# Kernel tuning notes

Hardware: AMD Instinct MI355X
Metric: run time of the kernel (lower is better)

Reference implementation:

```python
import jax, jax.numpy as jnp
import numpy as np

CONF = 0.25
IOU = 0.7
MAX_DET = 300
IMG_H = 1280
IMG_W = 1280
KPT_SHAPE = (17, 3)
MAX_NMS = 3000
BS = 16
N_ANCH = 33600  # (1280/8)^2 + (1280/16)^2 + (1280/32)^2


def setup_inputs() -> dict:
    key = jax.random.key(0)
    k1, k2, k3, k4 = jax.random.split(key, 4)
    # realistic YOLO head outputs: centers in image, positive w/h, conf in (0,1)
    cxy = jax.random.uniform(k1, (BS, 2, N_ANCH)) * jnp.array([IMG_W, IMG_H], jnp.float32).reshape(1, 2, 1)
    wh = jax.random.uniform(k2, (BS, 2, N_ANCH)) * 200.0 + 4.0
    conf = jax.random.uniform(k3, (BS, 1, N_ANCH))
    kpts = jax.random.uniform(k4, (BS, 51, N_ANCH)) * float(IMG_W)
    preds = jnp.concatenate([cxy, wh, conf, kpts], axis=1).astype(jnp.float32)
    return {"preds": preds}


def _pairwise_iou(boxes):
    # boxes: [M, 4] xyxy
    area = (boxes[:, 2] - boxes[:, 0]) * (boxes[:, 3] - boxes[:, 1])
    lt = jnp.maximum(boxes[:, None, :2], boxes[None, :, :2])
    rb = jnp.minimum(boxes[:, None, 2:], boxes[None, :, 2:])
    wh = jnp.clip(rb - lt, 0.0)
    inter = wh[..., 0] * wh[..., 1]
    return inter / (area[:, None] + area[None, :] - inter + 1e-9)


def _nms_keep(boxes, valid):
    # greedy NMS over score-descending boxes; returns bool keep mask [M]
    M = boxes.shape[0]
    idx = jnp.arange(M)
    supp = (_pairwise_iou(boxes) > IOU) & (idx[None, :] > idx[:, None])

    def body(i, keep):
        # row i suppresses later boxes only if it is itself kept
        return keep & ~(supp[i] & keep[i])

    return jax.lax.fori_loop(0, M, body, valid)


def _per_image(boxes_xywh, scores, kpts):
    # boxes_xywh: [N,4], scores: [N], kpts: [N,51]
    valid = scores > CONF
    masked = jnp.where(valid, scores, -1.0)
    order = jnp.argsort(-masked)[:MAX_NMS]  # top max_nms by score, desc
    b = boxes_xywh[order]
    sc = scores[order]
    kp = kpts[order]
    v = valid[order]
    # xywh -> xyxy with clip to image bounds
    cx, cy, w, h = b[:, 0], b[:, 1], b[:, 2], b[:, 3]
    x1 = jnp.clip(cx - w / 2, 0.0, IMG_W)
    y1 = jnp.clip(cy - h / 2, 0.0, IMG_H)
    x2 = jnp.clip(cx + w / 2, 0.0, IMG_W)
    y2 = jnp.clip(cy + h / 2, 0.0, IMG_H)
    bxy = jnp.stack([x1, y1, x2, y2], axis=-1)
    # faithful to original _clip_coords quirk: only channels 0 and 1 of the 51 clipped
    kp = kp.at[:, 0].set(jnp.clip(kp[:, 0], 0.0, IMG_W))
    kp = kp.at[:, 1].set(jnp.clip(kp[:, 1], 0.0, IMG_H))
    keep = _nms_keep(bxy, v)
    rank = jnp.cumsum(keep) - 1
    sel = keep & (rank < MAX_DET)
    tgt = jnp.where(sel, rank, MAX_DET)  # dropped rows scatter to slot MAX_DET (sliced off)
    ob = jnp.zeros((MAX_DET + 1, 4), bxy.dtype).at[tgt].set(jnp.where(sel[:, None], bxy, 0.0))[:MAX_DET]
    osc = jnp.zeros((MAX_DET + 1, 1), sc.dtype).at[tgt].set(jnp.where(sel[:, None], sc[:, None], 0.0))[:MAX_DET]
    okp = jnp.zeros((MAX_DET + 1, 51), kp.dtype).at[tgt].set(jnp.where(sel[:, None], kp, 0.0))[:MAX_DET]
    return ob, osc, okp


def reference(preds):
    bs = preds.shape[0]
    x = jnp.transpose(preds, (0, 2, 1))  # [bs, N, 56]
    ob, osc, okp = jax.vmap(_per_image)(x[..., :4], x[..., 4], x[..., 5:])
    return ob, osc, okp.reshape(bs, MAX_DET, *KPT_SHAPE)
```

## Files before the change

### kernel.cpp

```cpp
#include <hip/hip_runtime.h>
#include <stdint.h>

#define N_ANCH 33600
#define BS 16
#define NCH 56
#define MAX_NMS 3000
#define MAX_DET 300
#define CONF_T 0.25f
#define IOU_T 0.7f
#define IMG 1280.0f
#define NW 47
#define NBINS 4096
#define HIST_BINS 4097
#define S_STRIDE 4104
#define CAP 4096

#define OFF_CURS 0
#define OFF_KEPT (OFF_CURS + BS*NBINS*4)
#define ZERO_BYTES (OFF_KEPT + 64)
#define OFF_HIST  ZERO_BYTES
#define OFF_START (OFF_HIST + BS*S_STRIDE*4)
#define OFF_B     (OFF_START + BS*S_STRIDE*4)
#define OFF_M     (OFF_B + 64)
#define OFF_CAND  (OFF_M + 64)
#define OFF_SORT  (OFF_CAND + BS*CAP*8)
#define OFF_OIDX  (OFF_SORT + BS*CAP*8)
#define OFF_SC    (OFF_OIDX + BS*MAX_NMS*4)
#define OFF_BOX   (OFF_SC + BS*MAX_NMS*4)
#define OFF_SEL   (OFF_BOX + BS*MAX_NMS*16)

__device__ __forceinline__ int score_bucket(float c, uint32_t* bits_out) {
    if (!(c > CONF_T)) { *bits_out = 0u; return 0; }
    uint32_t bits = __float_as_uint(c);
    *bits_out = bits;
    int bucket = (int)(bits >> 12) - 0x3E800 + 1;
    bucket = bucket < 1 ? 1 : (bucket > NBINS ? NBINS : bucket);
    return bucket;
}

__global__ void k_histscan(const float* __restrict__ preds, int* __restrict__ hist,
                           int* __restrict__ start, int* __restrict__ Bthr,
                           int* __restrict__ Mout) {
    __shared__ int hl[HIST_BINS];
    __shared__ int part[256];
    __shared__ int suf[256];
    int b = blockIdx.x, t = threadIdx.x;
    for (int i = t; i < HIST_BINS; i += 1024) hl[i] = 0;
    __syncthreads();
    const float* conf = preds + (size_t)b * NCH * N_ANCH + 4 * N_ANCH;
    for (int a = t; a < N_ANCH; a += 1024) {
        uint32_t bits;
        int bucket = score_bucket(conf[a], &bits);
        if (bucket > 0) atomicAdd(&hl[bucket], 1);
    }
    __syncthreads();
    if (t < 256) {
        int s = 0;
        for (int k = 0; k < 16; k++) s += hl[1 + t * 16 + k];
        part[t] = s;
    }
    __syncthreads();
    if (t == 0) {
        int run = 0;
        for (int i = 255; i >= 0; i--) { suf[i] = run; run += part[i]; }
        if (run < MAX_NMS) { Bthr[b] = 1; Mout[b] = run; }
    }
    __syncthreads();
    if (t < 256) {
        int run = suf[t];
        bool maycross = (run < MAX_NMS) && (run + part[t] >= MAX_NMS);
        bool done = false;
        for (int k = 15; k >= 0; k--) {
            int bin = 1 + t * 16 + k;
            start[b * S_STRIDE + bin] = run;
            hist[b * S_STRIDE + bin] = hl[bin];
            run += hl[bin];
            if (maycross && !done && run >= MAX_NMS) {
                Bthr[b] = bin; Mout[b] = run; done = true;
            }
        }
    }
}

__global__ void k_scatter(const float* __restrict__ preds, const int* __restrict__ Bthr,
                          const int* __restrict__ start, int* __restrict__ curs,
                          unsigned long long* __restrict__ cand) {
    int g = blockIdx.x * blockDim.x + threadIdx.x;
    if (g >= BS * N_ANCH) return;
    int b = g / N_ANCH, a = g - b * N_ANCH;
    float c = preds[(size_t)b * NCH * N_ANCH + 4 * N_ANCH + a];
    uint32_t bits;
    int bucket = score_bucket(c, &bits);
    if (bucket > 0 && bucket >= Bthr[b]) {
        int pos = start[b * S_STRIDE + bucket] + atomicAdd(&curs[b * NBINS + (bucket - 1)], 1);
        if (pos < CAP)
            cand[b * CAP + pos] =
                ((unsigned long long)bits << 32) | (uint32_t)(~(uint32_t)a);
    }
}

__global__ void k_rank(const int* __restrict__ Bthr, const int* __restrict__ start,
                       const int* __restrict__ hist,
                       const unsigned long long* __restrict__ cand,
                       unsigned long long* __restrict__ sorted) {
    int wid = (blockIdx.x * blockDim.x + threadIdx.x) >> 6;
    int lane = threadIdx.x & 63;
    if (wid >= BS * NBINS) return;
    int b = wid >> 12;
    int bin = (wid & (NBINS - 1)) + 1;
    if (bin < Bthr[b]) return;
    int s = start[b * S_STRIDE + bin];
    if (s >= MAX_NMS) return;
    int n = hist[b * S_STRIDE + bin];
    if (n <= 0) return;
    if (s + n > CAP) n = CAP - s;
    const unsigned long long* seg = cand + b * CAP + s;
    unsigned long long* oseg = sorted + b * CAP + s;
    for (int e = lane; e < n; e += 64) {
        unsigned long long ke = seg[e];
        int r = 0;
        for (int j = 0; j < n; j++) r += (seg[j] > ke);
        oseg[r] = ke;
    }
}

__global__ void k_gather(const float* __restrict__ preds,
                         const unsigned long long* __restrict__ sorted,
                         const int* __restrict__ M,
                         int* __restrict__ oidx, float* __restrict__ sc_out,
                         float4* __restrict__ box_out) {
    int g = blockIdx.x * blockDim.x + threadIdx.x;
    if (g >= BS * MAX_NMS) return;
    int b = g / MAX_NMS, p = g - b * MAX_NMS;
    float score; float4 bx; int oi;
    if (p < M[b]) {
        unsigned long long key = sorted[b * CAP + p];
        const float* pr = preds + (size_t)b * NCH * N_ANCH;
        oi = (int)(~(uint32_t)key);
        score = __uint_as_float((uint32_t)(key >> 32));
        float cx = pr[0 * N_ANCH + oi], cy = pr[1 * N_ANCH + oi];
        float w  = pr[2 * N_ANCH + oi], h  = pr[3 * N_ANCH + oi];
        bx.x = fminf(fmaxf(cx - w * 0.5f, 0.f), IMG);
        bx.y = fminf(fmaxf(cy - h * 0.5f, 0.f), IMG);
        bx.z = fminf(fmaxf(cx + w * 0.5f, 0.f), IMG);
        bx.w = fminf(fmaxf(cy + h * 0.5f, 0.f), IMG);
    } else {
        oi = 0; score = -1.0f; bx = make_float4(0.f, 0.f, 0.f, 0.f);
    }
    oidx[b * MAX_NMS + p] = oi;
    sc_out[b * MAX_NMS + p] = score;
    box_out[b * MAX_NMS + p] = bx;
}

__device__ __forceinline__ float iou_pair(float4 bi, float ai, float4 bj) {
    float aj  = (bj.z - bj.x) * (bj.w - bj.y);
    float ltx = fmaxf(bi.x, bj.x), lty = fmaxf(bi.y, bj.y);
    float rbx = fminf(bi.z, bj.z), rby = fminf(bi.w, bj.w);
    float wx  = fmaxf(rbx - ltx, 0.f), wy = fmaxf(rby - lty, 0.f);
    float inter = wx * wy;
    return inter / (ai + aj - inter + 1e-9f);
}

__device__ __forceinline__ unsigned long long readlane64(unsigned long long v, int lane) {
    uint32_t lo = (uint32_t)v, hi = (uint32_t)(v >> 32);
    uint32_t rlo = __builtin_amdgcn_readlane(lo, lane);
    uint32_t rhi = __builtin_amdgcn_readlane(hi, lane);
    return ((unsigned long long)rhi << 32) | (unsigned long long)rlo;
}

__global__ void k_nms(const float4* __restrict__ box_ws, const float* __restrict__ sc_ws,
                      int* __restrict__ sel_slot, int* __restrict__ kept_count) {
    __shared__ float4 lbox[MAX_NMS];
    __shared__ float4 kbox[MAX_DET];
    __shared__ float  karea[MAX_DET];
    __shared__ unsigned long long pres[NW];
    __shared__ unsigned long long diag[64];
    __shared__ unsigned long long keptmask_sh;
    int b = blockIdx.x, t = threadIdx.x;
    if (t < NW) pres[t] = 0ull;
    __syncthreads();
    for (int j = t; j < MAX_NMS; j += 1024) {
        lbox[j] = box_ws[b * MAX_NMS + j];
        if (!(sc_ws[b * MAX_NMS + j] > CONF_T))
            atomicOr(&pres[j >> 6], 1ull << (j & 63));
    }
    __syncthreads();
    int kc = 0;
    for (int c = 0; c < NW && kc < MAX_DET; c++) {
        int base = c * 64;
        if (t < 64) diag[t] = 0ull;
        __syncthreads();
        {
            int jl = t >> 4, kk = t & 15;
            int j = base + jl;
            if (j < MAX_NMS && kc > 0) {
                float4 bj = lbox[j];
                bool sup = false;
                for (int kidx = kk; kidx < kc; kidx += 16) {
                    if (iou_pair(kbox[kidx], karea[kidx], bj) > IOU_T) { sup = true; break; }
                }
                if (sup) atomicOr(&pres[c], 1ull << jl);
            }
        }
        {
            int il = t >> 4;
            int j0 = (t & 15) * 4;
            int i = base + il;
            if (i < MAX_NMS) {
                float4 bi = lbox[i];
                float ai = (bi.z - bi.x) * (bi.w - bi.y);
                unsigned long long m = 0ull;
                for (int q = 0; q < 4; q++) {
                    int jl = j0 + q, j = base + jl;
                    if (j > i && j < MAX_NMS) {
                        if (iou_pair(bi, ai, lbox[j]) > IOU_T) m |= 1ull << jl;
                    }
                }
                if (m) atomicOr(&diag[il], m);
            }
        }
        __syncthreads();
        if (t < 64) {
            unsigned long long mydiag = diag[t];
            unsigned long long s = pres[c];
            unsigned long long keptm = 0ull;
            int room = MAX_DET - kc;
            int jmax = MAX_NMS - base; if (jmax > 64) jmax = 64;
            for (int bb = 0; bb < jmax; bb++) {
                if (!((s >> bb) & 1ull)) {
                    s |= readlane64(mydiag, bb);
                    keptm |= 1ull << bb;
                    if (--room == 0) break;
                }
            }
            if (t == 0) keptmask_sh = keptm;
        }
        __syncthreads();
        unsigned long long keptm = keptmask_sh;
        if (t < 64 && ((keptm >> t) & 1ull)) {
            int pos = kc + __popcll(keptm & ((1ull << t) - 1ull));
            float4 bx = lbox[base + t];
            kbox[pos] = bx;
            karea[pos] = (bx.z - bx.x) * (bx.w - bx.y);
            sel_slot[b * MAX_DET + pos] = base + t;
        }
        kc += __popcll(keptm);
        __syncthreads();
    }
    if (t == 0) kept_count[b] = kc;
}

__global__ void k_out(const float* __restrict__ preds, const float4* __restrict__ box_ws,
                      const float* __restrict__ sc_ws, const int* __restrict__ oidx,
                      const int* __restrict__ sel_slot, const int* __restrict__ kept_count,
                      float* __restrict__ out) {
    int g = blockIdx.x * blockDim.x + threadIdx.x;
    if (g >= BS * MAX_DET * 64) return;
    int det = g >> 6, lane = g & 63;
    int b = det / MAX_DET, r = det - b * MAX_DET;
    int kc = kept_count[b];
    float* ob  = out;
    float* osc = out + BS * MAX_DET * 4;
    float* okp = out + BS * MAX_DET * 5;
    if (r < kc) {
        int s = sel_slot[b * MAX_DET + r];
        if (lane < 4) {
            float4 bx = box_ws[b * MAX_NMS + s];
            float v = (lane == 0) ? bx.x : (lane == 1) ? bx.y : (lane == 2) ? bx.z : bx.w;
            ob[det * 4 + lane] = v;
        } else if (lane == 4) {
            osc[det] = sc_ws[b * MAX_NMS + s];
        } else if (lane < 56) {
            int k = lane - 5;
            int oi = oidx[b * MAX_NMS + s];
            float v = preds[(size_t)b * NCH * N_ANCH + (size_t)(5 + k) * N_ANCH + oi];
            if (k < 2) v = fminf(fmaxf(v, 0.f), IMG);
            okp[det * 51 + k] = v;
        }
    } else {
        if (lane < 4)       ob[det * 4 + lane] = 0.f;
        else if (lane == 4) osc[det] = 0.f;
        else if (lane < 56) okp[det * 51 + (lane - 5)] = 0.f;
    }
}

extern "C" void kernel_launch(void* const* d_in, const int* in_sizes, int n_in,
                              void* d_out, int out_size, void* d_ws, size_t ws_size,
                              hipStream_t stream) {
    const float* preds = (const float*)d_in[0];
    float* out = (float*)d_out;
    char* ws = (char*)d_ws;
    int* curs  = (int*)(ws + OFF_CURS);
    int* kept  = (int*)(ws + OFF_KEPT);
    int* hist  = (int*)(ws + OFF_HIST);
    int* start = (int*)(ws + OFF_START);
    int* Bthr  = (int*)(ws + OFF_B);
    int* M     = (int*)(ws + OFF_M);
    unsigned long long* cand   = (unsigned long long*)(ws + OFF_CAND);
    unsigned long long* sorted = (unsigned long long*)(ws + OFF_SORT);
    int* oidx = (int*)(ws + OFF_OIDX);
    float* sc = (float*)(ws + OFF_SC);
    float4* box = (float4*)(ws + OFF_BOX);
    int* sel = (int*)(ws + OFF_SEL);

    hipMemsetAsync(d_ws, 0, ZERO_BYTES, stream);
    k_histscan<<<BS, 1024, 0, stream>>>(preds, hist, start, Bthr, M);
    k_scatter<<<(BS * N_ANCH + 255) / 256, 256, 0, stream>>>(preds, Bthr, start, curs, cand);
    k_rank<<<(BS * NBINS * 64) / 256, 256, 0, stream>>>(Bthr, start, hist, cand, sorted);
    k_gather<<<(BS * MAX_NMS + 255) / 256, 256, 0, stream>>>(preds, sorted, M, oidx, sc, box);
    k_nms<<<BS, 1024, 0, stream>>>(box, sc, sel, kept);
    k_out<<<(BS * MAX_DET * 64 + 255) / 256, 256, 0, stream>>>(preds, box, sc, oidx, sel, kept, out);
}
```

Before: 259.9 us.

## Fuse top-k pipeline into three kernels with compacted bin worklist

Merges histogram, prefix scan and scatter into a single per-image block that keeps bin starts in shared memory. This removes the workspace memset and the global cursor atomics. The per-bin rank sort now walks a compacted worklist of non-empty bins and writes gathered boxes directly, instead of launching one wave per bin. NMS and output writing are also fused, which removes two more launches. The cost is less parallelism in the scatter phase, since only 16 blocks do that work.

```diff
diff --git a/kernel.cpp b/kernel.cpp
--- a/kernel.cpp
+++ b/kernel.cpp
@@ -12,22 +12,16 @@
 #define NW 47
 #define NBINS 4096
 #define HIST_BINS 4097
-#define S_STRIDE 4104
 #define CAP 4096
-
-#define OFF_CURS 0
-#define OFF_KEPT (OFF_CURS + BS*NBINS*4)
-#define ZERO_BYTES (OFF_KEPT + 64)
-#define OFF_HIST  ZERO_BYTES
-#define OFF_START (OFF_HIST + BS*S_STRIDE*4)
-#define OFF_B     (OFF_START + BS*S_STRIDE*4)
-#define OFF_M     (OFF_B + 64)
-#define OFF_CAND  (OFF_M + 64)
-#define OFF_SORT  (OFF_CAND + BS*CAP*8)
-#define OFF_OIDX  (OFF_SORT + BS*CAP*8)
-#define OFF_SC    (OFF_OIDX + BS*MAX_NMS*4)
-#define OFF_BOX   (OFF_SC + BS*MAX_NMS*4)
-#define OFF_SEL   (OFF_BOX + BS*MAX_NMS*16)
+#define WCAP 4096
+#define WC_STRIDE 16
+
+#define OFF_CAND 0
+#define OFF_WL   (OFF_CAND + BS*CAP*8)
+#define OFF_WC   (OFF_WL + BS*WCAP*4)
+#define OFF_OIDX (OFF_WC + BS*WC_STRIDE*4)
+#define OFF_SC   (OFF_OIDX + BS*MAX_NMS*4)
+#define OFF_BOX  (OFF_SC + BS*MAX_NMS*4)
 
 __device__ __forceinline__ int score_bucket(float c, uint32_t* bits_out) {
     if (!(c > CONF_T)) { *bits_out = 0u; return 0; }
@@ -38,13 +32,18 @@
     return bucket;
 }
 
-__global__ void k_histscan(const float* __restrict__ preds, int* __restrict__ hist,
-                           int* __restrict__ start, int* __restrict__ Bthr,
-                           int* __restrict__ Mout) {
+__global__ void k_phase1(const float* __restrict__ preds,
+                         unsigned long long* __restrict__ cand,
+                         unsigned int* __restrict__ wlist, int* __restrict__ wcount,
+                         int* __restrict__ oidx, float* __restrict__ sc_out,
+                         float4* __restrict__ box_out) {
     __shared__ int hl[HIST_BINS];
+    __shared__ int st[HIST_BINS];
     __shared__ int part[256];
     __shared__ int suf[256];
+    __shared__ int ldsB, ldsM, ldsWc;
     int b = blockIdx.x, t = threadIdx.x;
+    if (t == 0) { ldsWc = 0; }
     for (int i = t; i < HIST_BINS; i += 1024) hl[i] = 0;
     __syncthreads();
     const float* conf = preds + (size_t)b * NCH * N_ANCH + 4 * N_ANCH;
@@ -63,7 +62,7 @@
     if (t == 0) {
         int run = 0;
         for (int i = 255; i >= 0; i--) { suf[i] = run; run += part[i]; }
-        if (run < MAX_NMS) { Bthr[b] = 1; Mout[b] = run; }
+        if (run < MAX_NMS) { ldsB = 1; ldsM = run; }
     }
     __syncthreads();
     if (t < 256) {
@@ -72,84 +71,81 @@
         bool done = false;
         for (int k = 15; k >= 0; k--) {
             int bin = 1 + t * 16 + k;
-            start[b * S_STRIDE + bin] = run;
-            hist[b * S_STRIDE + bin] = hl[bin];
+            st[bin] = run;
             run += hl[bin];
-            if (maycross && !done && run >= MAX_NMS) {
-                Bthr[b] = bin; Mout[b] = run; done = true;
-            }
-        }
-    }
-}
-
-__global__ void k_scatter(const float* __restrict__ preds, const int* __restrict__ Bthr,
-                          const int* __restrict__ start, int* __restrict__ curs,
-                          unsigned long long* __restrict__ cand) {
-    int g = blockIdx.x * blockDim.x + threadIdx.x;
-    if (g >= BS * N_ANCH) return;
-    int b = g / N_ANCH, a = g - b * N_ANCH;
-    float c = preds[(size_t)b * NCH * N_ANCH + 4 * N_ANCH + a];
-    uint32_t bits;
-    int bucket = score_bucket(c, &bits);
-    if (bucket > 0 && bucket >= Bthr[b]) {
-        int pos = start[b * S_STRIDE + bucket] + atomicAdd(&curs[b * NBINS + (bucket - 1)], 1);
-        if (pos < CAP)
-            cand[b * CAP + pos] =
-                ((unsigned long long)bits << 32) | (uint32_t)(~(uint32_t)a);
-    }
-}
-
-__global__ void k_rank(const int* __restrict__ Bthr, const int* __restrict__ start,
-                       const int* __restrict__ hist,
-                       const unsigned long long* __restrict__ cand,
-                       unsigned long long* __restrict__ sorted) {
-    int wid = (blockIdx.x * blockDim.x + threadIdx.x) >> 6;
+            if (maycross && !done && run >= MAX_NMS) { ldsB = bin; ldsM = run; done = true; }
+        }
+    }
+    __syncthreads();
+    int B = ldsB, M = ldsM;
+    if (t < 256) {
+        for (int k = 0; k < 16; k++) {
+            int bin = 1 + t * 16 + k;
+            int c = hl[bin], s = st[bin];
+            if (c > 0 && bin >= B && s < MAX_NMS) {
+                int idx = atomicAdd(&ldsWc, 1);
+                wlist[b * WCAP + idx] = (unsigned int)s | ((unsigned int)c << 16);
+            }
+        }
+    }
+    __syncthreads();
+    for (int a = t; a < N_ANCH; a += 1024) {
+        uint32_t bits;
+        int bucket = score_bucket(conf[a], &bits);
+        if (bucket >= B && bucket > 0) {
+            int pos = atomicAdd(&st[bucket], 1);
+            if (pos < CAP)
+                cand[b * CAP + pos] =
+                    ((unsigned long long)bits << 32) | (uint32_t)(~(uint32_t)a);
+        }
+    }
+    for (int p = M + t; p < MAX_NMS; p += 1024) {
+        sc_out[b * MAX_NMS + p] = -1.0f;
+        box_out[b * MAX_NMS + p] = make_float4(0.f, 0.f, 0.f, 0.f);
+        oidx[b * MAX_NMS + p] = 0;
+    }
+    if (t == 0) wcount[b * WC_STRIDE] = ldsWc;
+}
+
+__global__ void k_rank2(const float* __restrict__ preds,
+                        const unsigned long long* __restrict__ cand,
+                        const unsigned int* __restrict__ wlist,
+                        const int* __restrict__ wcount,
+                        int* __restrict__ oidx, float* __restrict__ sc_out,
+                        float4* __restrict__ box_out) {
+    int b = blockIdx.x;
+    int wc = wcount[b * WC_STRIDE];
+    int wv = blockIdx.y * (blockDim.x >> 6) + (threadIdx.x >> 6);
     int lane = threadIdx.x & 63;
-    if (wid >= BS * NBINS) return;
-    int b = wid >> 12;
-    int bin = (wid & (NBINS - 1)) + 1;
-    if (bin < Bthr[b]) return;
-    int s = start[b * S_STRIDE + bin];
-    if (s >= MAX_NMS) return;
-    int n = hist[b * S_STRIDE + bin];
-    if (n <= 0) return;
-    if (s + n > CAP) n = CAP - s;
-    const unsigned long long* seg = cand + b * CAP + s;
-    unsigned long long* oseg = sorted + b * CAP + s;
-    for (int e = lane; e < n; e += 64) {
-        unsigned long long ke = seg[e];
-        int r = 0;
-        for (int j = 0; j < n; j++) r += (seg[j] > ke);
-        oseg[r] = ke;
-    }
-}
-
-__global__ void k_gather(const float* __restrict__ preds,
-                         const unsigned long long* __restrict__ sorted,
-                         const int* __restrict__ M,
-                         int* __restrict__ oidx, float* __restrict__ sc_out,
-                         float4* __restrict__ box_out) {
-    int g = blockIdx.x * blockDim.x + threadIdx.x;
-    if (g >= BS * MAX_NMS) return;
-    int b = g / MAX_NMS, p = g - b * MAX_NMS;
-    float score; float4 bx; int oi;
-    if (p < M[b]) {
-        unsigned long long key = sorted[b * CAP + p];
-        const float* pr = preds + (size_t)b * NCH * N_ANCH;
-        oi = (int)(~(uint32_t)key);
-        score = __uint_as_float((uint32_t)(key >> 32));
-        float cx = pr[0 * N_ANCH + oi], cy = pr[1 * N_ANCH + oi];
-        float w  = pr[2 * N_ANCH + oi], h  = pr[3 * N_ANCH + oi];
-        bx.x = fminf(fmaxf(cx - w * 0.5f, 0.f), IMG);
-        bx.y = fminf(fmaxf(cy - h * 0.5f, 0.f), IMG);
-        bx.z = fminf(fmaxf(cx + w * 0.5f, 0.f), IMG);
-        bx.w = fminf(fmaxf(cy + h * 0.5f, 0.f), IMG);
-    } else {
-        oi = 0; score = -1.0f; bx = make_float4(0.f, 0.f, 0.f, 0.f);
-    }
-    oidx[b * MAX_NMS + p] = oi;
-    sc_out[b * MAX_NMS + p] = score;
-    box_out[b * MAX_NMS + p] = bx;
+    const int wstride = gridDim.y * (blockDim.x >> 6);
+    const float* pr = preds + (size_t)b * NCH * N_ANCH;
+    for (int e = wv; e < wc; e += wstride) {
+        unsigned int ent = wlist[b * WCAP + e];
+        int s = (int)(ent & 0xffffu);
+        int n = (int)(ent >> 16);
+        if (s + n > CAP) n = CAP - s;
+        const unsigned long long* seg = cand + b * CAP + s;
+        for (int i = lane; i < n; i += 64) {
+            unsigned long long ke = seg[i];
+            int r = 0;
+            for (int j = 0; j < n; j++) r += (seg[j] > ke);
+            int pos = s + r;
+            if (pos < MAX_NMS) {
+                int oi = (int)(~(uint32_t)ke);
+                float score = __uint_as_float((uint32_t)(ke >> 32));
+                float cx = pr[0 * N_ANCH + oi], cy = pr[1 * N_ANCH + oi];
+                float w  = pr[2 * N_ANCH + oi], h  = pr[3 * N_ANCH + oi];
+                float4 bx;
+                bx.x = fminf(fmaxf(cx - w * 0.5f, 0.f), IMG);
+                bx.y = fminf(fmaxf(cy - h * 0.5f, 0.f), IMG);
+                bx.z = fminf(fmaxf(cx + w * 0.5f, 0.f), IMG);
+                bx.w = fminf(fmaxf(cy + h * 0.5f, 0.f), IMG);
+                oidx[b * MAX_NMS + pos] = oi;
+                sc_out[b * MAX_NMS + pos] = score;
+                box_out[b * MAX_NMS + pos] = bx;
+            }
+        }
+    }
 }
 
 __device__ __forceinline__ float iou_pair(float4 bi, float ai, float4 bj) {
@@ -168,11 +164,13 @@
     return ((unsigned long long)rhi << 32) | (unsigned long long)rlo;
 }
 
-__global__ void k_nms(const float4* __restrict__ box_ws, const float* __restrict__ sc_ws,
-                      int* __restrict__ sel_slot, int* __restrict__ kept_count) {
+__global__ void k_nms_out(const float* __restrict__ preds,
+                          const float4* __restrict__ box_ws, const float* __restrict__ sc_ws,
+                          const int* __restrict__ oidx_ws, float* __restrict__ out) {
     __shared__ float4 lbox[MAX_NMS];
     __shared__ float4 kbox[MAX_DET];
     __shared__ float  karea[MAX_DET];
+    __shared__ int    lsel[MAX_DET];
     __shared__ unsigned long long pres[NW];
     __shared__ unsigned long long diag[64];
     __shared__ unsigned long long keptmask_sh;
@@ -242,45 +240,38 @@
             float4 bx = lbox[base + t];
             kbox[pos] = bx;
             karea[pos] = (bx.z - bx.x) * (bx.w - bx.y);
-            sel_slot[b * MAX_DET + pos] = base + t;
+            lsel[pos] = base + t;
         }
         kc += __popcll(keptm);
         __syncthreads();
     }
-    if (t == 0) kept_count[b] = kc;
-}
-
-__global__ void k_out(const float* __restrict__ preds, const float4* __restrict__ box_ws,
-                      const float* __restrict__ sc_ws, const int* __restrict__ oidx,
-                      const int* __restrict__ sel_slot, const int* __restrict__ kept_count,
-                      float* __restrict__ out) {
-    int g = blockIdx.x * blockDim.x + threadIdx.x;
-    if (g >= BS * MAX_DET * 64) return;
-    int det = g >> 6, lane = g & 63;
-    int b = det / MAX_DET, r = det - b * MAX_DET;
-    int kc = kept_count[b];
     float* ob  = out;
     float* osc = out + BS * MAX_DET * 4;
     float* okp = out + BS * MAX_DET * 5;
-    if (r < kc) {
-        int s = sel_slot[b * MAX_DET + r];
-        if (lane < 4) {
-            float4 bx = box_ws[b * MAX_NMS + s];
-            float v = (lane == 0) ? bx.x : (lane == 1) ? bx.y : (lane == 2) ? bx.z : bx.w;
-            ob[det * 4 + lane] = v;
-        } else if (lane == 4) {
-            osc[det] = sc_ws[b * MAX_NMS + s];
-        } else if (lane < 56) {
-            int k = lane - 5;
-            int oi = oidx[b * MAX_NMS + s];
-            float v = preds[(size_t)b * NCH * N_ANCH + (size_t)(5 + k) * N_ANCH + oi];
-            if (k < 2) v = fminf(fmaxf(v, 0.f), IMG);
-            okp[det * 51 + k] = v;
-        }
-    } else {
-        if (lane < 4)       ob[det * 4 + lane] = 0.f;
-        else if (lane == 4) osc[det] = 0.f;
-        else if (lane < 56) okp[det * 51 + (lane - 5)] = 0.f;
+    const float* pr = preds + (size_t)b * NCH * N_ANCH;
+    for (int g = t; g < MAX_DET * 64; g += 1024) {
+        int r = g >> 6, lane = g & 63;
+        int det = b * MAX_DET + r;
+        if (r < kc) {
+            int s = lsel[r];
+            if (lane < 4) {
+                float4 bx = kbox[r];
+                float v = (lane == 0) ? bx.x : (lane == 1) ? bx.y : (lane == 2) ? bx.z : bx.w;
+                ob[det * 4 + lane] = v;
+            } else if (lane == 4) {
+                osc[det] = sc_ws[b * MAX_NMS + s];
+            } else if (lane < 56) {
+                int k = lane - 5;
+                int oi = oidx_ws[b * MAX_NMS + s];
+                float v = pr[(size_t)(5 + k) * N_ANCH + oi];
+                if (k < 2) v = fminf(fmaxf(v, 0.f), IMG);
+                okp[det * 51 + k] = v;
+            }
+        } else {
+            if (lane < 4)       ob[det * 4 + lane] = 0.f;
+            else if (lane == 4) osc[det] = 0.f;
+            else if (lane < 56) okp[det * 51 + (lane - 5)] = 0.f;
+        }
     }
 }
 
@@ -290,24 +281,14 @@
     const float* preds = (const float*)d_in[0];
     float* out = (float*)d_out;
     char* ws = (char*)d_ws;
-    int* curs  = (int*)(ws + OFF_CURS);
-    int* kept  = (int*)(ws + OFF_KEPT);
-    int* hist  = (int*)(ws + OFF_HIST);
-    int* start = (int*)(ws + OFF_START);
-    int* Bthr  = (int*)(ws + OFF_B);
-    int* M     = (int*)(ws + OFF_M);
-    unsigned long long* cand   = (unsigned long long*)(ws + OFF_CAND);
-    unsigned long long* sorted = (unsigned long long*)(ws + OFF_SORT);
+    unsigned long long* cand = (unsigned long long*)(ws + OFF_CAND);
+    unsigned int* wlist = (unsigned int*)(ws + OFF_WL);
+    int* wcount = (int*)(ws + OFF_WC);
     int* oidx = (int*)(ws + OFF_OIDX);
     float* sc = (float*)(ws + OFF_SC);
     float4* box = (float4*)(ws + OFF_BOX);
-    int* sel = (int*)(ws + OFF_SEL);
-
-    hipMemsetAsync(d_ws, 0, ZERO_BYTES, stream);
-    k_histscan<<<BS, 1024, 0, stream>>>(preds, hist, start, Bthr, M);
-    k_scatter<<<(BS * N_ANCH + 255) / 256, 256, 0, stream>>>(preds, Bthr, start, curs, cand);
-    k_rank<<<(BS * NBINS * 64) / 256, 256, 0, stream>>>(Bthr, start, hist, cand, sorted);
-    k_gather<<<(BS * MAX_NMS + 255) / 256, 256, 0, stream>>>(preds, sorted, M, oidx, sc, box);
-    k_nms<<<BS, 1024, 0, stream>>>(box, sc, sel, kept);
-    k_out<<<(BS * MAX_DET * 64 + 255) / 256, 256, 0, stream>>>(preds, box, sc, oidx, sel, kept, out);
-}
+
+    k_phase1<<<BS, 1024, 0, stream>>>(preds, cand, wlist, wcount, oidx, sc, box);
+    k_rank2<<<dim3(BS, 32), 256, 0, stream>>>(preds, cand, wlist, wcount, oidx, sc, box);
+    k_nms_out<<<BS, 1024, 0, stream>>>(preds, box, sc, oidx, out);
+}
```

Result: slower. 293.5 us (+12.9%).
